# Optimization experiments

Hardware: AMD Instinct MI355X
Metric: run time of the kernel (lower is better)

The kernel has to match this reference:

```python
import jax, jax.numpy as jnp
import numpy as np

N = 50000
E = 1_600_000
H = 4
IN_F = 256
OUT_F = 32
NEG_SLOPE = 0.2
EPS = 1e-8


def setup_inputs() -> dict:
    key = jax.random.key(0)
    k1, k2, k3, k4, k5 = jax.random.split(key, 5)
    x = jax.random.normal(k1, (N, IN_F), dtype=jnp.float32)
    edge_index = jax.random.randint(k2, (2, E), 0, N, dtype=jnp.int64)
    # Xavier-uniform-like scale for params
    wb = float(np.sqrt(6.0 / (IN_F + OUT_F)))
    ab = float(np.sqrt(6.0 / (OUT_F + 1)))
    W = jax.random.uniform(k3, (H, IN_F, OUT_F), dtype=jnp.float32, minval=-wb, maxval=wb)
    a_l = jax.random.uniform(k4, (H, OUT_F, 1), dtype=jnp.float32, minval=-ab, maxval=ab)
    a_r = jax.random.uniform(k5, (H, OUT_F, 1), dtype=jnp.float32, minval=-ab, maxval=ab)
    return {"x": x, "edge_index": edge_index, "W": W, "a_l": a_l, "a_r": a_r}


def reference(x, edge_index, W, a_l, a_r):
    n = x.shape[0]
    h = jnp.einsum('ni,hio->nho', x, W)                      # (N, H, O)
    attn_l = jnp.einsum('nho,hol->nh', h, a_l)               # (N, H)
    attn_r = jnp.einsum('nho,hol->nh', h, a_r)               # (N, H)
    src, dst = edge_index[0], edge_index[1]
    e = attn_l[src] + attn_r[dst]                            # (E, H)
    e = jnp.where(e >= 0, e, NEG_SLOPE * e)                  # leaky_relu
    # segment softmax over edges grouped by dst (global max, as in source)
    e_exp = jnp.exp(e - jnp.max(e))
    e_sum = jax.ops.segment_sum(e_exp, dst, num_segments=n)  # (N, H)
    alpha = e_exp / (e_sum[dst] + EPS)                       # (E, H)
    msg = h[src] * alpha[:, :, None]                         # (E, H, O)
    out = jax.ops.segment_sum(msg, dst, num_segments=n)      # (N, H, O)
    return out.reshape(n, H * OUT_F)                         # concat=True
```

## Files before the change

### kernel.cpp

```cpp
#include <hip/hip_runtime.h>

#define NN    50000
#define NE    1600000
#define FOUT  128
#define NCH   128
#define EPC   12500
#define NW    12500
#define NSPLIT 4
#define NRNG  12500
#define NWH   3125
#define CSTR  96
#define LOG2E 1.4426950408889634f

typedef short s16x8 __attribute__((ext_vector_type(8)));
typedef float f32x4 __attribute__((ext_vector_type(4)));

#define OFF_M      0u
#define OFF_DEGP   16u
#define OFF_SEGB   12516u
#define OFF_C8     112516u
#define OFF_CSR    1712516u
#define OFF_H      4112516u
#define OFF_ATTL   7312516u
#define OFF_ATTR   7512516u
#define OFF_BP     7712516u
#define OFF_BQ     7728900u

__device__ __forceinline__ unsigned short f2bf(float f) {
  unsigned u = __float_as_uint(f);
  u += 0x7FFFu + ((u >> 16) & 1u);
  return (unsigned short)(u >> 16);
}
__device__ __forceinline__ unsigned cvtpk(float lo, float hi) {
  unsigned r;
  asm("v_cvt_pk_bf16_f32 %0, %1, %2" : "=v"(r) : "v"(lo), "v"(hi));
  return r;
}
__device__ __forceinline__ unsigned enc_f32(float f) {
  unsigned u = __float_as_uint(f);
  return (u & 0x80000000u) ? ~u : (u | 0x80000000u);
}
__device__ __forceinline__ float dec_f32(unsigned u) {
  u = (u & 0x80000000u) ? (u & 0x7fffffffu) : ~u;
  return __uint_as_float(u);
}

__global__ __launch_bounds__(256) void k_repack(const float* __restrict__ W,
                                                unsigned* __restrict__ Bp) {
  const int f = blockIdx.x * 256 + threadIdx.x;
  const int s = f >> 9;
  const int c = (f >> 6) & 7;
  const int l = f & 63;
  const int hd = c >> 1;
  const int colw = (c & 1) * 16 + (l & 15);
  const int kb = s * 32 + (l >> 4) * 8;
  unsigned short t[8];
#pragma unroll
  for (int j = 0; j < 8; ++j)
    t[j] = f2bf(W[hd * 8192 + (kb + j) * 32 + colw]);
  uint4 o;
  o.x = (unsigned)t[0] | ((unsigned)t[1] << 16);
  o.y = (unsigned)t[2] | ((unsigned)t[3] << 16);
  o.z = (unsigned)t[4] | ((unsigned)t[5] << 16);
  o.w = (unsigned)t[6] | ((unsigned)t[7] << 16);
  reinterpret_cast<uint4*>(Bp)[f] = o;
}

__global__ __launch_bounds__(256) void k_repack2(const float* __restrict__ W,
                                                 const float* __restrict__ a_l,
                                                 const float* __restrict__ a_r,
                                                 unsigned* __restrict__ Bq) {
  const int f = blockIdx.x * 256 + threadIdx.x;
  const int s = f >> 6;
  const int l = f & 63;
  const int col = l & 15;
  const int kb = s * 32 + (l >> 4) * 8;
  unsigned short t[8];
  if (col < 8) {
    const int hd = col & 3;
    const float* av = (col < 4 ? a_l : a_r) + hd * 32;
#pragma unroll
    for (int j = 0; j < 8; ++j) {
      const float* wr = W + hd * 8192 + (size_t)(kb + j) * 32;
      float dot = 0.f;
#pragma unroll
      for (int o = 0; o < 32; ++o) dot = fmaf(wr[o], av[o], dot);
      t[j] = f2bf(dot * LOG2E);
    }
  } else {
#pragma unroll
    for (int j = 0; j < 8; ++j) t[j] = 0;
  }
  uint4 o;
  o.x = (unsigned)t[0] | ((unsigned)t[1] << 16);
  o.y = (unsigned)t[2] | ((unsigned)t[3] << 16);
  o.z = (unsigned)t[4] | ((unsigned)t[5] << 16);
  o.w = (unsigned)t[6] | ((unsigned)t[7] << 16);
  reinterpret_cast<uint4*>(Bq)[f] = o;
}

__global__ __launch_bounds__(256) void k_gemm(const float* __restrict__ x,
                                              const uint4* __restrict__ Bp,
                                              const uint4* __restrict__ Bq,
                                              unsigned short* __restrict__ h,
                                              float* __restrict__ attl,
                                              float* __restrict__ attr) {
  const int t = threadIdx.x;
  const int wid = t >> 6, l = t & 63;
  const int n0 = (blockIdx.x * 4 + wid) * 16;
  const int lrow = l & 15, g = l >> 4;
  int r0 = n0 + lrow; if (r0 >= NN) r0 = NN - 1;
  const float* x0 = x + (size_t)r0 * 256 + g * 8;
  f32x4 acc[8], acc9;
#pragma unroll
  for (int c = 0; c < 8; ++c) acc[c] = (f32x4){0.f, 0.f, 0.f, 0.f};
  acc9 = (f32x4){0.f, 0.f, 0.f, 0.f};
#pragma unroll
  for (int s = 0; s < 8; ++s) {
    const float4 u0 = *reinterpret_cast<const float4*>(x0 + s * 32);
    const float4 u1 = *reinterpret_cast<const float4*>(x0 + s * 32 + 4);
    union { s16x8 v; unsigned w[4]; } a;
    a.w[0] = cvtpk(u0.x, u0.y);
    a.w[1] = cvtpk(u0.z, u0.w);
    a.w[2] = cvtpk(u1.x, u1.y);
    a.w[3] = cvtpk(u1.z, u1.w);
#pragma unroll
    for (int c = 0; c < 8; ++c) {
      union { uint4 q; s16x8 v; } b;
      b.q = Bp[(s * 8 + c) * 64 + l];
      acc[c] = __builtin_amdgcn_mfma_f32_16x16x32_bf16(a.v, b.v, acc[c], 0, 0, 0);
    }
    union { uint4 q; s16x8 v; } b9;
    b9.q = Bq[s * 64 + l];
    acc9 = __builtin_amdgcn_mfma_f32_16x16x32_bf16(a.v, b9.v, acc9, 0, 0, 0);
  }
#pragma unroll
  for (int c = 0; c < 8; ++c) {
#pragma unroll
    for (int r = 0; r < 4; ++r) {
      const int na = n0 + g * 4 + r;
      if (na < NN) h[(size_t)na * FOUT + c * 16 + lrow] = f2bf(acc[c][r]);
    }
  }
  if (lrow < 8) {
    float* dst = (lrow < 4) ? attl : attr;
    const int hd = lrow & 3;
#pragma unroll
    for (int r = 0; r < 4; ++r) {
      const int na = n0 + g * 4 + r;
      if (na < NN) dst[na * 4 + hd] = acc9[r];
    }
  }
}

__global__ __launch_bounds__(512) void k_histA(const int* __restrict__ ei,
                                               unsigned* __restrict__ c8) {
  __shared__ unsigned lh[NWH];
  const int b = blockIdx.x, t = threadIdx.x;
  const int chunk = b >> 2, half = b & 3;
  const unsigned nlo = half * NRNG;
  for (int w = t; w < NWH; w += 512) lh[w] = 0u;
  __syncthreads();
  const int base = chunk * EPC;
  for (int k = t; k < EPC; k += 512) {
    const unsigned dl = (unsigned)ei[NE + base + k] - nlo;
    if (dl < (unsigned)NRNG) atomicAdd(&lh[dl >> 2], 1u << ((dl & 3) * 8));
  }
  __syncthreads();
  unsigned* dst = c8 + (size_t)chunk * NW + half * NWH;
  for (int w = t; w < NWH; w += 512) dst[w] = lh[w];
}

__global__ __launch_bounds__(256) void k_cscan1(unsigned* __restrict__ c8,
                                                unsigned* __restrict__ segb) {
  const int b = blockIdx.x;
  const int seg = b / 49;
  const int w = (b % 49) * 256 + threadIdx.x;
  if (w >= NW) return;
  unsigned R = 0;
  const int c0 = seg * 16;
#pragma unroll
  for (int c = 0; c < 16; ++c) {
    const unsigned tt = c8[(size_t)(c0 + c) * NW + w];
    c8[(size_t)(c0 + c) * NW + w] = R;
    R += tt;
  }
  segb[seg * NW + w] = R;
}

__global__ __launch_bounds__(256) void k_cscan2(unsigned* __restrict__ segb,
                                                unsigned* __restrict__ degp) {
  const int w = blockIdx.x * 256 + threadIdx.x;
  if (w >= NW) return;
  unsigned R = 0;
#pragma unroll
  for (int s = 0; s < 8; ++s) {
    const unsigned tt = segb[s * NW + w];
    segb[s * NW + w] = R;
    R += tt;
  }
  degp[w] = R;
}

__global__ __launch_bounds__(512) void k_rank(const int* __restrict__ ei,
                                              const unsigned* __restrict__ c8,
                                              const unsigned* __restrict__ segb,
                                              unsigned short* __restrict__ csr) {
  __shared__ unsigned lh[NWH];
  const int b = blockIdx.x, t = threadIdx.x;
  const int chunk = b >> 2, half = b & 3;
  const unsigned nlo = half * NRNG;
  const unsigned* c8b = c8 + (size_t)chunk * NW + half * NWH;
  const unsigned* sgb = segb + (size_t)(chunk >> 4) * NW + half * NWH;
  for (int w = t; w < NWH; w += 512) lh[w] = c8b[w] + sgb[w];
  __syncthreads();
  const int base = chunk * EPC;
  for (int k = t; k < EPC; k += 512) {
    const int d = ei[NE + base + k];
    const unsigned dl = (unsigned)d - nlo;
    if (dl < (unsigned)NRNG) {
      const int s = ei[base + k];
      const int sh = (dl & 3) * 8;
      const unsigned old = atomicAdd(&lh[dl >> 2], 1u << sh);
      csr[(size_t)d * CSTR + ((old >> sh) & 0xffu)] = (unsigned short)s;
    }
  }
}

__global__ __launch_bounds__(256) void k_agg(const unsigned short* __restrict__ csr,
                                             const unsigned* __restrict__ degp,
                                             const float* __restrict__ attl,
                                             const float* __restrict__ attr,
                                             const unsigned* __restrict__ hpk,
                                             float* __restrict__ outac,
                                             float* __restrict__ wsbuf,
                                             unsigned* __restrict__ Mslot) {
  __shared__ float wmax[4];
  const int t = threadIdx.x;
  const int wid = t >> 6, l = t & 63;
  const int q = l & 31;
  const int n = blockIdx.x * 8 + wid * 2 + (l >> 5);
  const int hd = q >> 3;
  const float ar = attr[n * 4 + hd];
  const int deg = (int)((degp[n >> 2] >> ((n & 3) * 8)) & 0xffu);
  const unsigned lo = (unsigned)n * CSTR;
  int mdeg = max(deg, __shfl_xor(deg, 32));
  const int nb = (mdeg + 3) >> 2;
  float acc0 = 0.f, acc1 = 0.f, acc2 = 0.f, acc3 = 0.f, wsum = 0.f;
  float mlk = -3.4e38f;

  float alA[4]; uint2 hvA[4];
#define LOADB(BASE, alB, hvB)                                              \
  {                                                                        \
    _Pragma("unroll")                                                      \
    for (int j = 0; j < 4; ++j) {                                          \
      const int i = (BASE) + j;                                            \
      const unsigned idx = lo + (unsigned)((i < deg) ? i : 0);             \
      const unsigned s = csr[idx];                                         \
      const float a = attl[s * 4 + hd];                                    \
      alB[j] = (i < deg) ? a : -1e30f;                                     \
      hvB[j] = *reinterpret_cast<const uint2*>(&hpk[(size_t)s * 64 + q * 2]); \
    }                                                                      \
  }
#define COMPUTE(alB, hvB)                                                  \
  {                                                                        \
    _Pragma("unroll")                                                      \
    for (int j = 0; j < 4; ++j) {                                          \
      const float v = alB[j] + ar;                                         \
      const float lk = fmaxf(v, 0.2f * v);                                 \
      mlk = fmaxf(mlk, lk);                                                \
      const float w = __builtin_amdgcn_exp2f(lk);                          \
      wsum += w;                                                           \
      acc0 = fmaf(w, __uint_as_float(hvB[j].x << 16), acc0);               \
      acc1 = fmaf(w, __uint_as_float(hvB[j].x & 0xffff0000u), acc1);       \
      acc2 = fmaf(w, __uint_as_float(hvB[j].y << 16), acc2);               \
      acc3 = fmaf(w, __uint_as_float(hvB[j].y & 0xffff0000u), acc3);       \
    }                                                                      \
  }
  if (nb > 0) {
    LOADB(0, alA, hvA);
    for (int b = 1; b < nb; ++b) {
      float alB[4]; uint2 hvB[4];
      LOADB(b * 4, alB, hvB);
      COMPUTE(alA, hvA);
#pragma unroll
      for (int j = 0; j < 4; ++j) { alA[j] = alB[j]; hvA[j] = hvB[j]; }
    }
    COMPUTE(alA, hvA);
  }
  float4 o;
  o.x = acc0; o.y = acc1; o.z = acc2; o.w = acc3;
  *reinterpret_cast<float4*>(&outac[(size_t)n * FOUT + q * 4]) = o;
  if ((q & 7) == 0) wsbuf[n * 4 + hd] = wsum;
#pragma unroll
  for (int m = 1; m < 64; m <<= 1) mlk = fmaxf(mlk, __shfl_xor(mlk, m));
  if (l == 0) wmax[wid] = mlk;
  __syncthreads();
  if (t == 0) {
    const float m = fmaxf(fmaxf(wmax[0], wmax[1]), fmaxf(wmax[2], wmax[3]));
    atomicMax(Mslot, enc_f32(m));
  }
#undef LOADB
#undef COMPUTE
}

__global__ __launch_bounds__(256) void k_fix(const float* __restrict__ wsbuf,
                                             const unsigned* __restrict__ Mslot,
                                             float4* __restrict__ outv) {
  const int f = blockIdx.x * 256 + threadIdx.x;
  const int n = f >> 5, c = f & 31, hd = c >> 3;
  const float eps2 = 1e-8f * __builtin_amdgcn_exp2f(dec_f32(*Mslot));
  const float w = wsbuf[n * 4 + hd];
  const float inv = 1.f / (w + eps2);
  float4 a = outv[f];
  a.x *= inv; a.y *= inv; a.z *= inv; a.w *= inv;
  outv[f] = a;
}

extern "C" void kernel_launch(void* const* d_in, const int* in_sizes, int n_in,
                              void* d_out, int out_size, void* d_ws, size_t ws_size,
                              hipStream_t stream) {
  const float* x   = (const float*)d_in[0];
  const int*   ei  = (const int*)d_in[1];
  const float* W   = (const float*)d_in[2];
  const float* a_l = (const float*)d_in[3];
  const float* a_r = (const float*)d_in[4];
  float* out = (float*)d_out;
  unsigned* ws = (unsigned*)d_ws;

  unsigned* Mslot   = ws + OFF_M;
  unsigned* degp    = ws + OFF_DEGP;
  unsigned* segb    = ws + OFF_SEGB;
  unsigned* c8      = ws + OFF_C8;
  float*    wsbuf   = (float*)(ws + OFF_C8);
  unsigned short* csr = (unsigned short*)(ws + OFF_CSR);
  unsigned short* h = (unsigned short*)(ws + OFF_H);
  float*    attl    = (float*)(ws + OFF_ATTL);
  float*    attr    = (float*)(ws + OFF_ATTR);
  unsigned* Bp      = ws + OFF_BP;
  unsigned* Bq      = ws + OFF_BQ;

  hipMemsetAsync(Mslot, 0, 16 * sizeof(unsigned), stream);

  k_repack <<<16, 256, 0, stream>>>(W, Bp);
  k_repack2<<<2, 256, 0, stream>>>(W, a_l, a_r, Bq);
  k_gemm   <<<(NN + 63) / 64, 256, 0, stream>>>(x, (const uint4*)Bp, (const uint4*)Bq,
                                                h, attl, attr);
  k_histA  <<<NCH * NSPLIT, 512, 0, stream>>>(ei, c8);
  k_cscan1 <<<392, 256, 0, stream>>>(c8, segb);
  k_cscan2 <<<49, 256, 0, stream>>>(segb, degp);
  k_rank   <<<NCH * NSPLIT, 512, 0, stream>>>(ei, c8, segb, csr);
  k_agg    <<<NN / 8, 256, 0, stream>>>(csr, degp, attl, attr,
                                        (const unsigned*)h, out, wsbuf, Mslot);
  k_fix    <<<6250, 256, 0, stream>>>(wsbuf, Mslot, (float4*)out);
}
```

Before: 310.5 us.

## Split h and attention arrays into per-head planes for head-partitioned aggregation

The GEMM now writes h, attl and attr in head-major planes: each pair of heads forms a contiguous 64-byte row per node, and the attention scalars are stored per head. The aggregation kernel is re-partitioned so each block handles one head-pair slice, with 16 lanes per node gathering 4-byte chunks. The goal is a smaller per-head gather working set, so source rows of one plane fit better in cache. In exchange, the CSR index list is read once per head slice, per-edge gathers become smaller transactions, and more blocks are launched. Nontemporal stores and loads are also added for the output and the weight sums.

```diff
diff --git a/kernel.cpp b/kernel.cpp
--- a/kernel.cpp
+++ b/kernel.cpp
@@ -14,6 +14,7 @@
 
 typedef short s16x8 __attribute__((ext_vector_type(8)));
 typedef float f32x4 __attribute__((ext_vector_type(4)));
+typedef float f32x2 __attribute__((ext_vector_type(2)));
 
 #define OFF_M      0u
 #define OFF_DEGP   16u
@@ -139,7 +140,8 @@
 #pragma unroll
     for (int r = 0; r < 4; ++r) {
       const int na = n0 + g * 4 + r;
-      if (na < NN) h[(size_t)na * FOUT + c * 16 + lrow] = f2bf(acc[c][r]);
+      if (na < NN)
+        h[((size_t)(c >> 1) * NN + na) * 32 + (c & 1) * 16 + lrow] = f2bf(acc[c][r]);
     }
   }
   if (lrow < 8) {
@@ -148,7 +150,7 @@
 #pragma unroll
     for (int r = 0; r < 4; ++r) {
       const int na = n0 + g * 4 + r;
-      if (na < NN) dst[na * 4 + hd] = acc9[r];
+      if (na < NN) dst[(size_t)hd * NN + na] = acc9[r];
     }
   }
 }
@@ -237,19 +239,22 @@
                                              unsigned* __restrict__ Mslot) {
   __shared__ float wmax[4];
   const int t = threadIdx.x;
+  const int q = blockIdx.x & 3;
   const int wid = t >> 6, l = t & 63;
-  const int q = l & 31;
-  const int n = blockIdx.x * 8 + wid * 2 + (l >> 5);
-  const int hd = q >> 3;
-  const float ar = attr[n * 4 + hd];
+  const int g2 = l >> 4, l16 = l & 15;
+  const int n = (blockIdx.x >> 2) * 16 + wid * 4 + g2;
+  const float ar = attr[(size_t)q * NN + n];
   const int deg = (int)((degp[n >> 2] >> ((n & 3) * 8)) & 0xffu);
   const unsigned lo = (unsigned)n * CSTR;
-  int mdeg = max(deg, __shfl_xor(deg, 32));
+  const float* atlq = attl + (size_t)q * NN;
+  const unsigned* hq = hpk + (size_t)q * NN * 16;
+  int mdeg = max(deg, __shfl_xor(deg, 16));
+  mdeg = max(mdeg, __shfl_xor(mdeg, 32));
   const int nb = (mdeg + 3) >> 2;
-  float acc0 = 0.f, acc1 = 0.f, acc2 = 0.f, acc3 = 0.f, wsum = 0.f;
+  float acc0 = 0.f, acc1 = 0.f, wsum = 0.f;
   float mlk = -3.4e38f;
 
-  float alA[4]; uint2 hvA[4];
+  float alA[4]; unsigned hvA[4];
 #define LOADB(BASE, alB, hvB)                                              \
   {                                                                        \
     _Pragma("unroll")                                                      \
@@ -257,9 +262,9 @@
       const int i = (BASE) + j;                                            \
       const unsigned idx = lo + (unsigned)((i < deg) ? i : 0);             \
       const unsigned s = csr[idx];                                         \
-      const float a = attl[s * 4 + hd];                                    \
+      const float a = atlq[s];                                             \
       alB[j] = (i < deg) ? a : -1e30f;                                     \
-      hvB[j] = *reinterpret_cast<const uint2*>(&hpk[(size_t)s * 64 + q * 2]); \
+      hvB[j] = hq[(size_t)s * 16 + l16];                                   \
     }                                                                      \
   }
 #define COMPUTE(alB, hvB)                                                  \
@@ -271,16 +276,14 @@
       mlk = fmaxf(mlk, lk);                                                \
       const float w = __builtin_amdgcn_exp2f(lk);                          \
       wsum += w;                                                           \
-      acc0 = fmaf(w, __uint_as_float(hvB[j].x << 16), acc0);               \
-      acc1 = fmaf(w, __uint_as_float(hvB[j].x & 0xffff0000u), acc1);       \
-      acc2 = fmaf(w, __uint_as_float(hvB[j].y << 16), acc2);               \
-      acc3 = fmaf(w, __uint_as_float(hvB[j].y & 0xffff0000u), acc3);       \
+      acc0 = fmaf(w, __uint_as_float(hvB[j] << 16), acc0);                 \
+      acc1 = fmaf(w, __uint_as_float(hvB[j] & 0xffff0000u), acc1);         \
     }                                                                      \
   }
   if (nb > 0) {
     LOADB(0, alA, hvA);
     for (int b = 1; b < nb; ++b) {
-      float alB[4]; uint2 hvB[4];
+      float alB[4]; unsigned hvB[4];
       LOADB(b * 4, alB, hvB);
       COMPUTE(alA, hvA);
 #pragma unroll
@@ -288,10 +291,10 @@
     }
     COMPUTE(alA, hvA);
   }
-  float4 o;
-  o.x = acc0; o.y = acc1; o.z = acc2; o.w = acc3;
-  *reinterpret_cast<float4*>(&outac[(size_t)n * FOUT + q * 4]) = o;
-  if ((q & 7) == 0) wsbuf[n * 4 + hd] = wsum;
+  f32x2 o2; o2.x = acc0; o2.y = acc1;
+  __builtin_nontemporal_store(o2,
+      reinterpret_cast<f32x2*>(outac) + (size_t)n * 64 + q * 16 + l16);
+  if (l16 == 0) __builtin_nontemporal_store(wsum, &wsbuf[(size_t)q * NN + n]);
 #pragma unroll
   for (int m = 1; m < 64; m <<= 1) mlk = fmaxf(mlk, __shfl_xor(mlk, m));
   if (l == 0) wmax[wid] = mlk;
@@ -306,15 +309,15 @@
 
 __global__ __launch_bounds__(256) void k_fix(const float* __restrict__ wsbuf,
                                              const unsigned* __restrict__ Mslot,
-                                             float4* __restrict__ outv) {
+                                             f32x4* __restrict__ outv) {
   const int f = blockIdx.x * 256 + threadIdx.x;
-  const int n = f >> 5, c = f & 31, hd = c >> 3;
+  const int n = f >> 5, c = f & 31, q = c >> 3;
   const float eps2 = 1e-8f * __builtin_amdgcn_exp2f(dec_f32(*Mslot));
-  const float w = wsbuf[n * 4 + hd];
+  const float w = wsbuf[(size_t)q * NN + n];
   const float inv = 1.f / (w + eps2);
-  float4 a = outv[f];
+  f32x4 a = __builtin_nontemporal_load(&outv[f]);
   a.x *= inv; a.y *= inv; a.z *= inv; a.w *= inv;
-  outv[f] = a;
+  __builtin_nontemporal_store(a, &outv[f]);
 }
 
 extern "C" void kernel_launch(void* const* d_in, const int* in_sizes, int n_in,
@@ -350,7 +353,7 @@
   k_cscan1 <<<392, 256, 0, stream>>>(c8, segb);
   k_cscan2 <<<49, 256, 0, stream>>>(segb, degp);
   k_rank   <<<NCH * NSPLIT, 512, 0, stream>>>(ei, c8, segb, csr);
-  k_agg    <<<NN / 8, 256, 0, stream>>>(csr, degp, attl, attr,
-                                        (const unsigned*)h, out, wsbuf, Mslot);
-  k_fix    <<<6250, 256, 0, stream>>>(wsbuf, Mslot, (float4*)out);
-}
+  k_agg    <<<12500, 256, 0, stream>>>(csr, degp, attl, attr,
+                                       (const unsigned*)h, out, wsbuf, Mslot);
+  k_fix    <<<6250, 256, 0, stream>>>(wsbuf, Mslot, (f32x4*)out);
+}
```

Measured after the change: 366.8 us. 1.18x slower.

## Fold softmax normalisation into aggregation and switch h/attention to head-major layout

Applied to the files above, without the earlier changes.

Removes the global-max tracking, the atomicMax, the memset and the separate normalisation pass. The aggregation kernel now divides by the per-head weight sum directly and writes the output once with nontemporal stores. The GEMM writes h, attl and attr in head-major order, so each aggregation block gathers from a single head's smaller array, which should improve cache locality. The two repack kernels are merged into one launch. The catch is that logits are no longer shifted by the maximum and eps is no longer scaled, so this relies on the exp2 values staying in range.

```diff
diff --git a/kernel.cpp b/kernel.cpp
--- a/kernel.cpp
+++ b/kernel.cpp
@@ -15,7 +15,6 @@
 typedef short s16x8 __attribute__((ext_vector_type(8)));
 typedef float f32x4 __attribute__((ext_vector_type(4)));
 
-#define OFF_M      0u
 #define OFF_DEGP   16u
 #define OFF_SEGB   12516u
 #define OFF_C8     112516u
@@ -36,67 +35,58 @@
   asm("v_cvt_pk_bf16_f32 %0, %1, %2" : "=v"(r) : "v"(lo), "v"(hi));
   return r;
 }
-__device__ __forceinline__ unsigned enc_f32(float f) {
-  unsigned u = __float_as_uint(f);
-  return (u & 0x80000000u) ? ~u : (u | 0x80000000u);
-}
-__device__ __forceinline__ float dec_f32(unsigned u) {
-  u = (u & 0x80000000u) ? (u & 0x7fffffffu) : ~u;
-  return __uint_as_float(u);
-}
 
 __global__ __launch_bounds__(256) void k_repack(const float* __restrict__ W,
-                                                unsigned* __restrict__ Bp) {
-  const int f = blockIdx.x * 256 + threadIdx.x;
-  const int s = f >> 9;
-  const int c = (f >> 6) & 7;
-  const int l = f & 63;
-  const int hd = c >> 1;
-  const int colw = (c & 1) * 16 + (l & 15);
-  const int kb = s * 32 + (l >> 4) * 8;
+                                                const float* __restrict__ a_l,
+                                                const float* __restrict__ a_r,
+                                                unsigned* __restrict__ Bp,
+                                                unsigned* __restrict__ Bq) {
   unsigned short t[8];
-#pragma unroll
-  for (int j = 0; j < 8; ++j)
-    t[j] = f2bf(W[hd * 8192 + (kb + j) * 32 + colw]);
-  uint4 o;
-  o.x = (unsigned)t[0] | ((unsigned)t[1] << 16);
-  o.y = (unsigned)t[2] | ((unsigned)t[3] << 16);
-  o.z = (unsigned)t[4] | ((unsigned)t[5] << 16);
-  o.w = (unsigned)t[6] | ((unsigned)t[7] << 16);
-  reinterpret_cast<uint4*>(Bp)[f] = o;
-}
-
-__global__ __launch_bounds__(256) void k_repack2(const float* __restrict__ W,
-                                                 const float* __restrict__ a_l,
-                                                 const float* __restrict__ a_r,
-                                                 unsigned* __restrict__ Bq) {
-  const int f = blockIdx.x * 256 + threadIdx.x;
-  const int s = f >> 6;
-  const int l = f & 63;
-  const int col = l & 15;
-  const int kb = s * 32 + (l >> 4) * 8;
-  unsigned short t[8];
-  if (col < 8) {
-    const int hd = col & 3;
-    const float* av = (col < 4 ? a_l : a_r) + hd * 32;
-#pragma unroll
-    for (int j = 0; j < 8; ++j) {
-      const float* wr = W + hd * 8192 + (size_t)(kb + j) * 32;
-      float dot = 0.f;
-#pragma unroll
-      for (int o = 0; o < 32; ++o) dot = fmaf(wr[o], av[o], dot);
-      t[j] = f2bf(dot * LOG2E);
-    }
+  if (blockIdx.x < 16) {
+    const int f = blockIdx.x * 256 + threadIdx.x;
+    const int s = f >> 9;
+    const int c = (f >> 6) & 7;
+    const int l = f & 63;
+    const int hd = c >> 1;
+    const int colw = (c & 1) * 16 + (l & 15);
+    const int kb = s * 32 + (l >> 4) * 8;
+#pragma unroll
+    for (int j = 0; j < 8; ++j)
+      t[j] = f2bf(W[hd * 8192 + (kb + j) * 32 + colw]);
+    uint4 o;
+    o.x = (unsigned)t[0] | ((unsigned)t[1] << 16);
+    o.y = (unsigned)t[2] | ((unsigned)t[3] << 16);
+    o.z = (unsigned)t[4] | ((unsigned)t[5] << 16);
+    o.w = (unsigned)t[6] | ((unsigned)t[7] << 16);
+    reinterpret_cast<uint4*>(Bp)[f] = o;
   } else {
-#pragma unroll
-    for (int j = 0; j < 8; ++j) t[j] = 0;
-  }
-  uint4 o;
-  o.x = (unsigned)t[0] | ((unsigned)t[1] << 16);
-  o.y = (unsigned)t[2] | ((unsigned)t[3] << 16);
-  o.z = (unsigned)t[4] | ((unsigned)t[5] << 16);
-  o.w = (unsigned)t[6] | ((unsigned)t[7] << 16);
-  reinterpret_cast<uint4*>(Bq)[f] = o;
+    const int f = (blockIdx.x - 16) * 256 + threadIdx.x;
+    const int s = f >> 6;
+    const int l = f & 63;
+    const int col = l & 15;
+    const int kb = s * 32 + (l >> 4) * 8;
+    if (col < 8) {
+      const int hd = col & 3;
+      const float* av = (col < 4 ? a_l : a_r) + hd * 32;
+#pragma unroll
+      for (int j = 0; j < 8; ++j) {
+        const float* wr = W + hd * 8192 + (size_t)(kb + j) * 32;
+        float dot = 0.f;
+#pragma unroll
+        for (int o = 0; o < 32; ++o) dot = fmaf(wr[o], av[o], dot);
+        t[j] = f2bf(dot * LOG2E);
+      }
+    } else {
+#pragma unroll
+      for (int j = 0; j < 8; ++j) t[j] = 0;
+    }
+    uint4 o;
+    o.x = (unsigned)t[0] | ((unsigned)t[1] << 16);
+    o.y = (unsigned)t[2] | ((unsigned)t[3] << 16);
+    o.z = (unsigned)t[4] | ((unsigned)t[5] << 16);
+    o.w = (unsigned)t[6] | ((unsigned)t[7] << 16);
+    reinterpret_cast<uint4*>(Bq)[f] = o;
+  }
 }
 
 __global__ __launch_bounds__(256) void k_gemm(const float* __restrict__ x,
@@ -139,7 +129,8 @@
 #pragma unroll
     for (int r = 0; r < 4; ++r) {
       const int na = n0 + g * 4 + r;
-      if (na < NN) h[(size_t)na * FOUT + c * 16 + lrow] = f2bf(acc[c][r]);
+      if (na < NN)
+        h[((size_t)(c >> 1) * NN + na) * 32 + (c & 1) * 16 + lrow] = f2bf(acc[c][r]);
     }
   }
   if (lrow < 8) {
@@ -148,7 +139,7 @@
 #pragma unroll
     for (int r = 0; r < 4; ++r) {
       const int na = n0 + g * 4 + r;
-      if (na < NN) dst[na * 4 + hd] = acc9[r];
+      if (na < NN) dst[(size_t)hd * NN + na] = acc9[r];
     }
   }
 }
@@ -227,27 +218,29 @@
   }
 }
 
-__global__ __launch_bounds__(256) void k_agg(const unsigned short* __restrict__ csr,
+__global__ __launch_bounds__(128) void k_agg(const unsigned short* __restrict__ csr,
                                              const unsigned* __restrict__ degp,
                                              const float* __restrict__ attl,
                                              const float* __restrict__ attr,
                                              const unsigned* __restrict__ hpk,
-                                             float* __restrict__ outac,
-                                             float* __restrict__ wsbuf,
-                                             unsigned* __restrict__ Mslot) {
-  __shared__ float wmax[4];
+                                             float* __restrict__ out) {
   const int t = threadIdx.x;
-  const int wid = t >> 6, l = t & 63;
-  const int q = l & 31;
-  const int n = blockIdx.x * 8 + wid * 2 + (l >> 5);
-  const int hd = q >> 3;
-  const float ar = attr[n * 4 + hd];
+  const int q = blockIdx.x & 3;
+  const int l = t & 63;
+  const int grp = l >> 3, l8 = l & 7;
+  const int wid = t >> 6;
+  const int n = (blockIdx.x >> 2) * 16 + wid * 8 + grp;
+  const float ar = attr[(size_t)q * NN + n];
   const int deg = (int)((degp[n >> 2] >> ((n & 3) * 8)) & 0xffu);
   const unsigned lo = (unsigned)n * CSTR;
-  int mdeg = max(deg, __shfl_xor(deg, 32));
+  const float* atlq = attl + (size_t)q * NN;
+  const uint2* hq2 = reinterpret_cast<const uint2*>(hpk + (size_t)q * NN * 16);
+  int mdeg = deg;
+  mdeg = max(mdeg, __shfl_xor(mdeg, 8));
+  mdeg = max(mdeg, __shfl_xor(mdeg, 16));
+  mdeg = max(mdeg, __shfl_xor(mdeg, 32));
   const int nb = (mdeg + 3) >> 2;
   float acc0 = 0.f, acc1 = 0.f, acc2 = 0.f, acc3 = 0.f, wsum = 0.f;
-  float mlk = -3.4e38f;
 
   float alA[4]; uint2 hvA[4];
 #define LOADB(BASE, alB, hvB)                                              \
@@ -257,9 +250,9 @@
       const int i = (BASE) + j;                                            \
       const unsigned idx = lo + (unsigned)((i < deg) ? i : 0);             \
       const unsigned s = csr[idx];                                         \
-      const float a = attl[s * 4 + hd];                                    \
+      const float a = atlq[s];                                             \
       alB[j] = (i < deg) ? a : -1e30f;                                     \
-      hvB[j] = *reinterpret_cast<const uint2*>(&hpk[(size_t)s * 64 + q * 2]); \
+      hvB[j] = hq2[(size_t)s * 8 + l8];                                    \
     }                                                                      \
   }
 #define COMPUTE(alB, hvB)                                                  \
@@ -268,7 +261,6 @@
     for (int j = 0; j < 4; ++j) {                                          \
       const float v = alB[j] + ar;                                         \
       const float lk = fmaxf(v, 0.2f * v);                                 \
-      mlk = fmaxf(mlk, lk);                                                \
       const float w = __builtin_amdgcn_exp2f(lk);                          \
       wsum += w;                                                           \
       acc0 = fmaf(w, __uint_as_float(hvB[j].x << 16), acc0);               \
@@ -288,33 +280,13 @@
     }
     COMPUTE(alA, hvA);
   }
-  float4 o;
-  o.x = acc0; o.y = acc1; o.z = acc2; o.w = acc3;
-  *reinterpret_cast<float4*>(&outac[(size_t)n * FOUT + q * 4]) = o;
-  if ((q & 7) == 0) wsbuf[n * 4 + hd] = wsum;
-#pragma unroll
-  for (int m = 1; m < 64; m <<= 1) mlk = fmaxf(mlk, __shfl_xor(mlk, m));
-  if (l == 0) wmax[wid] = mlk;
-  __syncthreads();
-  if (t == 0) {
-    const float m = fmaxf(fmaxf(wmax[0], wmax[1]), fmaxf(wmax[2], wmax[3]));
-    atomicMax(Mslot, enc_f32(m));
-  }
+  const float inv = 1.f / (wsum + 1e-8f);
+  f32x4 o;
+  o.x = acc0 * inv; o.y = acc1 * inv; o.z = acc2 * inv; o.w = acc3 * inv;
+  __builtin_nontemporal_store(o,
+      reinterpret_cast<f32x4*>(out + (size_t)n * FOUT + q * 32 + l8 * 4));
 #undef LOADB
 #undef COMPUTE
-}
-
-__global__ __launch_bounds__(256) void k_fix(const float* __restrict__ wsbuf,
-                                             const unsigned* __restrict__ Mslot,
-                                             float4* __restrict__ outv) {
-  const int f = blockIdx.x * 256 + threadIdx.x;
-  const int n = f >> 5, c = f & 31, hd = c >> 3;
-  const float eps2 = 1e-8f * __builtin_amdgcn_exp2f(dec_f32(*Mslot));
-  const float w = wsbuf[n * 4 + hd];
-  const float inv = 1.f / (w + eps2);
-  float4 a = outv[f];
-  a.x *= inv; a.y *= inv; a.z *= inv; a.w *= inv;
-  outv[f] = a;
 }
 
 extern "C" void kernel_launch(void* const* d_in, const int* in_sizes, int n_in,
@@ -328,11 +300,9 @@
   float* out = (float*)d_out;
   unsigned* ws = (unsigned*)d_ws;
 
-  unsigned* Mslot   = ws + OFF_M;
   unsigned* degp    = ws + OFF_DEGP;
   unsigned* segb    = ws + OFF_SEGB;
   unsigned* c8      = ws + OFF_C8;
-  float*    wsbuf   = (float*)(ws + OFF_C8);
   unsigned short* csr = (unsigned short*)(ws + OFF_CSR);
   unsigned short* h = (unsigned short*)(ws + OFF_H);
   float*    attl    = (float*)(ws + OFF_ATTL);
@@ -340,17 +310,13 @@
   unsigned* Bp      = ws + OFF_BP;
   unsigned* Bq      = ws + OFF_BQ;
 
-  hipMemsetAsync(Mslot, 0, 16 * sizeof(unsigned), stream);
-
-  k_repack <<<16, 256, 0, stream>>>(W, Bp);
-  k_repack2<<<2, 256, 0, stream>>>(W, a_l, a_r, Bq);
+  k_repack <<<18, 256, 0, stream>>>(W, a_l, a_r, Bp, Bq);
   k_gemm   <<<(NN + 63) / 64, 256, 0, stream>>>(x, (const uint4*)Bp, (const uint4*)Bq,
                                                 h, attl, attr);
   k_histA  <<<NCH * NSPLIT, 512, 0, stream>>>(ei, c8);
   k_cscan1 <<<392, 256, 0, stream>>>(c8, segb);
   k_cscan2 <<<49, 256, 0, stream>>>(segb, degp);
   k_rank   <<<NCH * NSPLIT, 512, 0, stream>>>(ei, c8, segb, csr);
-  k_agg    <<<NN / 8, 256, 0, stream>>>(csr, degp, attl, attr,
-                                        (const unsigned*)h, out, wsbuf, Mslot);
-  k_fix    <<<6250, 256, 0, stream>>>(wsbuf, Mslot, (float4*)out);
-}
+  k_agg    <<<12500, 128, 0, stream>>>(csr, degp, attl, attr,
+                                       (const unsigned*)h, out);
+}
```

Result: no change. 308.1 us (-0.7%).
